# Kernel optimization log

Hardware: AMD Instinct MI355X
Metric: run time of the kernel (lower is better)

Reference implementation:

```python
import jax, jax.numpy as jnp
import numpy as np

P = 113          # modulus; eq_token = P, vocab = P + 1
D_MODEL = 1024
D_MLP = 4096
BATCH = 16384


def setup_inputs() -> dict:
    key = jax.random.key(0)
    ks = jax.random.split(key, 9)
    return {
        "a": jax.random.randint(ks[0], (BATCH,), 0, P, dtype=jnp.int64 if jax.config.jax_enable_x64 else jnp.int32),
        "b": jax.random.randint(ks[1], (BATCH,), 0, P, dtype=jnp.int64 if jax.config.jax_enable_x64 else jnp.int32),
        "token_embed": jax.random.normal(ks[2], (P + 1, D_MODEL), dtype=jnp.float32),
        "pos_embed": jax.random.normal(ks[3], (3, D_MODEL), dtype=jnp.float32),
        "W_in_w": jax.random.normal(ks[4], (D_MLP, D_MODEL), dtype=jnp.float32) * (1.0 / np.sqrt(D_MODEL)),
        "W_in_b": jax.random.normal(ks[5], (D_MLP,), dtype=jnp.float32) * 0.02,
        "W_out_w": jax.random.normal(ks[6], (D_MODEL, D_MLP), dtype=jnp.float32) * (1.0 / np.sqrt(D_MLP)),
        "W_out_b": jax.random.normal(ks[7], (D_MODEL,), dtype=jnp.float32) * 0.02,
        "unembed_w": jax.random.normal(ks[8], (P, D_MODEL), dtype=jnp.float32) * (1.0 / np.sqrt(D_MODEL)),
    }


def reference(a, b, token_embed, pos_embed, W_in_w, W_in_b, W_out_w, W_out_b, unembed_w):
    # tokens: (batch, 3) = [a, b, eq]
    eq = jnp.full_like(a, P)
    tokens = jnp.stack([a, b, eq], axis=1)
    # embed + positional: (batch, 3, d_model)
    x = token_embed[tokens] + pos_embed[None, :, :]
    # FNet-style mixing: FFT over seq (axis 1), then over d_model (axis 2), real part
    wave = jnp.fft.fft(jnp.fft.fft(x, axis=1), axis=2).real.astype(x.dtype)
    x = x + wave
    # MLP with residual
    h = jax.nn.relu(jnp.einsum('bsd,md->bsm', x, W_in_w) + W_in_b)
    x = x + jnp.einsum('bsm,dm->bsd', h, W_out_w) + W_out_b
    # unembed only the '=' position (index 2)
    logits = jnp.einsum('bd,vd->bv', x[:, 2, :], unembed_w)
    return logits
```

## Files before the change

kernel.cpp:

```cpp
#include <hip/hip_runtime.h>

typedef __attribute__((ext_vector_type(4))) float f32x4;
typedef __attribute__((ext_vector_type(8))) short short8;
typedef __attribute__((ext_vector_type(4))) unsigned short us4;

#define PMOD 113
#define NPAIR 12769
#define DM 1024
#define DMLP 4096
#define NBATCH 16384
#define SQRT3_2 0.86602540378443865f
#define CSTEP 6.1359231515425649e-3f
#define NZ 8
#define HPELEMS (228 * 4224)

__device__ __forceinline__ short f2bf(float x) {
    unsigned int u = __builtin_bit_cast(unsigned int, x);
    u += 0x7FFFu + ((u >> 16) & 1u);
    return (short)(u >> 16);
}
__device__ __forceinline__ float bf2f(short s) {
    return __builtin_bit_cast(float, (unsigned int)(unsigned short)s << 16);
}
__device__ __forceinline__ void cvt16(const float* p, short8& o0, short8& o1) {
    #pragma unroll
    for (int c4 = 0; c4 < 4; ++c4) {
        f32x4 v = *(const f32x4*)(p + c4 * 4);
        #pragma unroll
        for (int e = 0; e < 4; ++e) {
            short s = f2bf(v[e]);
            if (c4 < 2) o0[c4 * 4 + e] = s; else o1[(c4 - 2) * 4 + e] = s;
        }
    }
}

__global__ __launch_bounds__(256) void k_prep(
    unsigned short* __restrict__ Fb, unsigned short* __restrict__ V2b,
    unsigned short* __restrict__ Wob, unsigned short* __restrict__ Wib,
    unsigned short* __restrict__ Ub,
    const float* __restrict__ E, const float* __restrict__ pos,
    const float* __restrict__ Wo, const float* __restrict__ Wi,
    const float* __restrict__ U)
{
    __shared__ float smem[64 * 65];
    const int blk = blockIdx.x, tid = threadIdx.x;

    if (blk < 1024) {
        const int f = blk;
        for (int k = tid; k < DM; k += 256) {
            float v;
            if (k <= 512) v = cosf((float)((f * k) & 1023) * CSTEP);
            else          v = sinf((float)((f * (k - 512)) & 1023) * CSTEP);
            Fb[f * DM + k] = (unsigned short)f2bf(v);
        }
    } else if (blk < 1252) {
        const int t = blk - 1024;
        if (t >= 226) {
            for (int k = tid; k < DM; k += 256) V2b[t * DM + k] = 0;
            return;
        }
        float* vc = smem;
        float* vs = smem + 1024;
        if (t < PMOD) {
            const float* e = E + t * DM;
            const float* e2 = E + PMOD * DM;
            for (int d = tid; d < DM; d += 256) {
                float e2v = e2[d] + pos[2 * DM + d];
                vc[d] = e[d] + pos[d] - 0.5f * pos[DM + d] - 0.5f * e2v;
                vs[d] = SQRT3_2 * (pos[DM + d] - e2v);
            }
        } else {
            const float* e = E + (t - PMOD) * DM;
            for (int d = tid; d < DM; d += 256) {
                float x = e[d];
                vc[d] = -0.5f * x;
                vs[d] = SQRT3_2 * x;
            }
        }
        __syncthreads();
        for (int k = tid; k < DM; k += 256) {
            float o;
            if (k == 0)        o = vc[0];
            else if (k < 512)  o = vc[k] + vc[1024 - k];
            else if (k == 512) o = vc[512];
            else               o = vs[k - 512] - vs[1536 - k];
            V2b[t * DM + k] = (unsigned short)f2bf(o);
        }
    } else if (blk < 2276) {
        const int idx = blk - 1252;
        const int m0 = (idx & 63) * 64;
        const int d0 = (idx >> 6) * 64;
        float (*tile)[65] = (float(*)[65])smem;
        #pragma unroll
        for (int it = 0; it < 16; ++it) {
            int i2 = tid + it * 256;
            int r = i2 >> 6, c = i2 & 63;
            tile[c][r] = Wo[(d0 + r) * DMLP + m0 + c];
        }
        __syncthreads();
        #pragma unroll
        for (int it = 0; it < 16; ++it) {
            int i2 = tid + it * 256;
            int r = i2 >> 6, c = i2 & 63;
            Wob[(m0 + r) * DM + d0 + c] = (unsigned short)f2bf(tile[r][c]);
        }
    } else if (blk < 3300) {
        const int eb = (blk - 2276) * 4096 + tid * 16;
        short8 o0, o1;
        cvt16(Wi + eb, o0, o1);
        *(short8*)&Wib[eb] = o0;
        *(short8*)&Wib[eb + 8] = o1;
    } else {
        const int eb = (blk - 3300) * 4096 + tid * 16;
        if (eb < PMOD * DM) {
            short8 o0, o1;
            cvt16(U + eb, o0, o1);
            *(short8*)&Ub[eb] = o0;
            *(short8*)&Ub[eb + 8] = o1;
        }
    }
}

template<int MODE>
__device__ __forceinline__ void mfma_body(
    int n0, int row0, int kbeg, int kend, int Arows,
    unsigned short* __restrict__ C1, float* __restrict__ C2f,
    const unsigned short* __restrict__ A, const unsigned short* __restrict__ B1,
    const unsigned short* __restrict__ B2,
    const float* __restrict__ E, const float* __restrict__ pos,
    const float* __restrict__ bo, short* sA, short* sB)
{
    const int tid = threadIdx.x;
    const int sr = tid >> 2, sq = (tid & 3) * 16;
    const int lane = tid & 63, w = tid >> 6;
    const int wr = w >> 1, wc = w & 1;
    const int lr = lane & 15, lg = lane >> 4;

    const unsigned short* Ab = (row0 + sr < Arows) ? (A + (row0 + sr) * DM) : nullptr;
    const unsigned short* Bb;
    {
        int n = n0 + sr;
        if (MODE == 1) {
            if (n < 4096) Bb = B1 + n * DM;
            else if (n - 4096 < PMOD) Bb = B2 + (n - 4096) * DM;
            else Bb = nullptr;
        } else {
            Bb = B1 + n * DM;
        }
    }

    f32x4 acc[2][2];
    #pragma unroll
    for (int i = 0; i < 2; ++i)
        #pragma unroll
        for (int j = 0; j < 2; ++j) acc[i][j] = 0.f;

    for (int k0 = kbeg; k0 < kend; k0 += 64) {
        short8 a0, a1, b0, b1;
        if (Ab) { a0 = ((const short8*)(Ab + k0 + sq))[0];
                  a1 = ((const short8*)(Ab + k0 + sq))[1]; }
        else { a0 = 0; a1 = 0; }
        if (Bb) { b0 = ((const short8*)(Bb + k0 + sq))[0];
                  b1 = ((const short8*)(Bb + k0 + sq))[1]; }
        else { b0 = 0; b1 = 0; }
        if (k0 != kbeg) __syncthreads();
        *(short8*)&sA[sr * 72 + sq] = a0;
        *(short8*)&sA[sr * 72 + sq + 8] = a1;
        *(short8*)&sB[sr * 72 + sq] = b0;
        *(short8*)&sB[sr * 72 + sq + 8] = b1;
        __syncthreads();

        #pragma unroll
        for (int ks = 0; ks < 2; ++ks) {
            short8 af[2], bfr[2];
            #pragma unroll
            for (int i = 0; i < 2; ++i)
                af[i] = *(const short8*)&sA[(wr * 32 + i * 16 + lr) * 72 + ks * 32 + lg * 8];
            #pragma unroll
            for (int j = 0; j < 2; ++j)
                bfr[j] = *(const short8*)&sB[(wc * 32 + j * 16 + lr) * 72 + ks * 32 + lg * 8];
            #pragma unroll
            for (int i = 0; i < 2; ++i)
                #pragma unroll
                for (int j = 0; j < 2; ++j)
                    acc[i][j] = __builtin_amdgcn_mfma_f32_16x16x32_bf16(af[i], bfr[j], acc[i][j], 0, 0, 0);
        }
    }

    #pragma unroll
    for (int i = 0; i < 2; ++i) {
        #pragma unroll
        for (int q = 0; q < 4; ++q) {
            int r = row0 + wr * 32 + i * 16 + lg * 4 + q;
            #pragma unroll
            for (int j = 0; j < 2; ++j) {
                int cg = n0 + wc * 32 + j * 16 + lr;
                float v = acc[i][j][q];
                if (MODE == 0) {
                    if (r < 228) {
                        if (r < PMOD) v += E[PMOD * DM + cg] + pos[2 * DM + cg];
                        if (r == 227) v += bo[cg];
                        C1[r * DM + cg] = (unsigned short)f2bf(v);
                    }
                } else if (MODE == 1) {
                    if (r < 228) C2f[r * 4224 + cg] = v;
                } else {
                    if (r < 128) C1[r * DMLP + cg] = (unsigned short)f2bf(v);
                }
            }
        }
    }
}

__global__ __launch_bounds__(256) void k_m02(
    unsigned short* __restrict__ Tb, unsigned short* __restrict__ Mb,
    const unsigned short* __restrict__ V2b, const unsigned short* __restrict__ Fb,
    const unsigned short* __restrict__ Ub, const unsigned short* __restrict__ Wob,
    const float* __restrict__ E, const float* __restrict__ pos,
    const float* __restrict__ bo)
{
    __shared__ short sA[64 * 72];
    __shared__ short sB[64 * 72];
    const int blk = blockIdx.x;
    if (blk < 64) {
        mfma_body<0>((blk & 15) * 64, (blk >> 4) * 64, 0, DM, 228, Tb, nullptr,
                     V2b, Fb, nullptr, E, pos, bo, sA, sB);
    } else {
        int i = blk - 64;
        mfma_body<2>((i & 63) * 64, (i >> 6) * 64, 0, DM, PMOD, Mb, nullptr,
                     Ub, Wob, nullptr, nullptr, nullptr, nullptr, sA, sB);
    }
}

__global__ __launch_bounds__(256) void k_m1(
    float* __restrict__ Hp,
    const unsigned short* __restrict__ Tb, const unsigned short* __restrict__ Wib,
    const unsigned short* __restrict__ Ub)
{
    __shared__ short sA[64 * 72];
    __shared__ short sB[64 * 72];
    const int kbeg = blockIdx.z * 256;
    mfma_body<1>(blockIdx.x * 64, blockIdx.y * 64, kbeg, kbeg + 256, 228,
                 nullptr, Hp + (size_t)blockIdx.z * HPELEMS,
                 Tb, Wib, Ub, nullptr, nullptr, nullptr, sA, sB);
}

__global__ __launch_bounds__(256) void k_hred(
    unsigned short* __restrict__ Hb, float* __restrict__ L,
    const float* __restrict__ Hp, const float* __restrict__ bi)
{
    const int e = (blockIdx.x * 256 + threadIdx.x) * 4;
    if (e >= HPELEMS) return;
    f32x4 s = *(const f32x4*)(Hp + e);
    #pragma unroll
    for (int z = 1; z < 4; ++z) s += *(const f32x4*)(Hp + (size_t)z * HPELEMS + e);
    unsigned int row = (unsigned)e / 4224u;
    unsigned int col = (unsigned)e - row * 4224u;
    if (col < 4096) {
        if (row < PMOD) s += *(const f32x4*)(bi + col);
        us4 o;
        #pragma unroll
        for (int j = 0; j < 4; ++j) o[j] = (unsigned short)f2bf(s[j]);
        *(us4*)&Hb[row * DMLP + col] = o;
    } else {
        *(f32x4*)&L[row * 128 + (col - 4096)] = s;
    }
}

__global__ __launch_bounds__(256) void k_pair_gemm(
    unsigned short* __restrict__ LTp,
    const unsigned short* __restrict__ Hb,
    const unsigned short* __restrict__ Mb,
    const float* __restrict__ L)
{
    __shared__ short sH[128 * 72];
    __shared__ short sM[128 * 72];

    const int tid = threadIdx.x;
    const int p0 = blockIdx.x * 128;
    const int z = blockIdx.y;
    const int kbeg = z * 512;
    const bool slice0 = (z == 0);

    const int hr = tid >> 1, kh = (tid & 1) * 32;
    const unsigned int pc = (unsigned)min(p0 + hr, NPAIR - 1);
    const unsigned int a_r = pc / 113u;
    const unsigned int b_r = pc - a_r * 113u;
    const unsigned short* pHA = Hb + a_r * DMLP + kbeg + kh;
    const unsigned short* pHB = Hb + (PMOD + b_r) * DMLP + kbeg + kh;
    const unsigned short* pM  = Mb + hr * DMLP + kbeg + kh;

    const int lane = tid & 63, w = tid >> 6;
    const int wr = w >> 1, wc = w & 1;
    const int lr = lane & 15, lg = lane >> 4;

    f32x4 acc[4][4];
    #pragma unroll
    for (int i = 0; i < 4; ++i)
        #pragma unroll
        for (int j = 0; j < 4; ++j) acc[i][j] = 0.f;

    short8 rA[4], rB[4], rM[4];
    #pragma unroll
    for (int c = 0; c < 4; ++c) {
        rA[c] = *(const short8*)(pHA + c * 8);
        rB[c] = *(const short8*)(pHB + c * 8);
        rM[c] = *(const short8*)(pM + c * 8);
    }

    #pragma unroll 1
    for (int t = 0; t < 8; ++t) {
        short8 u[4];
        #pragma unroll
        for (int c = 0; c < 4; ++c)
            #pragma unroll
            for (int e = 0; e < 8; ++e)
                u[c][e] = f2bf(fmaxf(bf2f(rA[c][e]) + bf2f(rB[c][e]), 0.f));

        if (t) __syncthreads();
        #pragma unroll
        for (int c = 0; c < 4; ++c) {
            *(short8*)&sH[hr * 72 + kh + c * 8] = u[c];
            *(short8*)&sM[hr * 72 + kh + c * 8] = rM[c];
        }
        __syncthreads();

        if (t < 7) {
            #pragma unroll
            for (int c = 0; c < 4; ++c) {
                rA[c] = *(const short8*)(pHA + (t + 1) * 64 + c * 8);
                rB[c] = *(const short8*)(pHB + (t + 1) * 64 + c * 8);
                rM[c] = *(const short8*)(pM + (t + 1) * 64 + c * 8);
            }
        }

        #pragma unroll
        for (int ks = 0; ks < 2; ++ks) {
            short8 af[4], bf[4];
            #pragma unroll
            for (int i = 0; i < 4; ++i)
                af[i] = *(const short8*)&sH[(wr * 64 + i * 16 + lr) * 72 + ks * 32 + lg * 8];
            #pragma unroll
            for (int j = 0; j < 4; ++j)
                bf[j] = *(const short8*)&sM[(wc * 64 + j * 16 + lr) * 72 + ks * 32 + lg * 8];
            #pragma unroll
            for (int i = 0; i < 4; ++i)
                #pragma unroll
                for (int j = 0; j < 4; ++j)
                    acc[i][j] = __builtin_amdgcn_mfma_f32_16x16x32_bf16(af[i], bf[j], acc[i][j], 0, 0, 0);
        }
    }

    const float* Lb0 = L + PMOD * 128;
    const float* Lc = L + 227 * 128;
    #pragma unroll
    for (int i = 0; i < 4; ++i) {
        #pragma unroll
        for (int q = 0; q < 4; ++q) {
            int p = p0 + wr * 64 + i * 16 + lg * 4 + q;
            if (p >= NPAIR) continue;
            unsigned int pa = (unsigned)p / 113u;
            unsigned int pb = (unsigned)p - pa * 113u;
            unsigned short* dst = LTp + ((size_t)p * NZ + z) * 128;
            const float* La = L + pa * 128;
            const float* Lb = Lb0 + pb * 128;
            #pragma unroll
            for (int j = 0; j < 4; ++j) {
                int col = wc * 64 + j * 16 + lr;
                float val = acc[i][j][q];
                if (slice0) val += La[col] + Lb[col] + Lc[col];
                dst[col] = (unsigned short)f2bf(val);
            }
        }
    }
}

__global__ __launch_bounds__(256) void k_gather(
    float* __restrict__ out, const unsigned short* __restrict__ LTp,
    const int* __restrict__ a, const int* __restrict__ b)
{
    const int tid = threadIdx.x;
    const int elem = blockIdx.x * 16 + (tid >> 4);
    const int t16 = tid & 15;
    const int v0 = t16 * 8;
    if (v0 > 112) return;
    unsigned int pair = (unsigned)a[elem] * 113u + (unsigned)b[elem];
    const unsigned short* src = LTp + (size_t)pair * (NZ * 128) + v0;
    float s[8];
    #pragma unroll
    for (int e = 0; e < 8; ++e) s[e] = 0.f;
    #pragma unroll
    for (int z = 0; z < NZ; ++z) {
        short8 vv = *(const short8*)(src + z * 128);
        #pragma unroll
        for (int e = 0; e < 8; ++e) s[e] += bf2f(vv[e]);
    }
    float* o = out + (size_t)elem * PMOD + v0;
    const int nv = (v0 + 8 <= PMOD) ? 8 : (PMOD - v0);
    for (int e = 0; e < nv; ++e) o[e] = s[e];
}

extern "C" void kernel_launch(void* const* d_in, const int* in_sizes, int n_in,
                              void* d_out, int out_size, void* d_ws, size_t ws_size,
                              hipStream_t stream)
{
    const int*   a   = (const int*)d_in[0];
    const int*   b   = (const int*)d_in[1];
    const float* E   = (const float*)d_in[2];
    const float* pos = (const float*)d_in[3];
    const float* Wi  = (const float*)d_in[4];
    const float* bi  = (const float*)d_in[5];
    const float* Wo  = (const float*)d_in[6];
    const float* bo  = (const float*)d_in[7];
    const float* U   = (const float*)d_in[8];
    float* out = (float*)d_out;

    unsigned short* Fb  = (unsigned short*)d_ws;
    unsigned short* V2b = Fb + 1024 * 1024;
    unsigned short* Tb  = V2b + 228 * 1024;
    unsigned short* Hb  = Tb + 228 * 1024;
    unsigned short* Wob = Hb + 228 * 4096;
    unsigned short* Mb  = Wob + 4096 * 1024;
    unsigned short* Wib = Mb + 128 * 4096;
    unsigned short* Ub  = Wib + 4096 * 1024;
    unsigned short* LTp = Ub + 116 * 1024;
    float* L  = (float*)(LTp + (size_t)12800 * NZ * 128);
    float* Hp = L + 228 * 128;

    k_prep<<<3329, 256, 0, stream>>>(Fb, V2b, Wob, Wib, Ub, E, pos, Wo, Wi, U);
    k_m02<<<192, 256, 0, stream>>>(Tb, Mb, V2b, Fb, Ub, Wob, E, pos, bo);
    k_m1<<<dim3(66, 4, 4), 256, 0, stream>>>(Hp, Tb, Wib, Ub);
    k_hred<<<(HPELEMS / 4 + 255) / 256, 256, 0, stream>>>(Hb, L, Hp, bi);
    k_pair_gemm<<<dim3(100, NZ), 256, 0, stream>>>(LTp, Hb, Mb, L);
    k_gather<<<NBATCH / 16, 256, 0, stream>>>(out, LTp, a, b);

    (void)in_sizes; (void)n_in; (void)out_size; (void)ws_size;
}
```

Baseline: 171.6 us.

## Load M operand directly to registers, double-buffer H tile, truncate bf16 conversion

```diff
diff --git a/kernel.cpp b/kernel.cpp
--- a/kernel.cpp
+++ b/kernel.cpp
@@ -3,6 +3,7 @@
 typedef __attribute__((ext_vector_type(4))) float f32x4;
 typedef __attribute__((ext_vector_type(8))) short short8;
 typedef __attribute__((ext_vector_type(4))) unsigned short us4;
+typedef __attribute__((ext_vector_type(4))) unsigned int u32x4;
 
 #define PMOD 113
 #define NPAIR 12769
@@ -273,8 +274,7 @@
     const unsigned short* __restrict__ Mb,
     const float* __restrict__ L)
 {
-    __shared__ short sH[128 * 72];
-    __shared__ short sM[128 * 72];
+    __shared__ short sH[2][128 * 72];
 
     const int tid = threadIdx.x;
     const int p0 = blockIdx.x * 128;
@@ -288,66 +288,77 @@
     const unsigned int b_r = pc - a_r * 113u;
     const unsigned short* pHA = Hb + a_r * DMLP + kbeg + kh;
     const unsigned short* pHB = Hb + (PMOD + b_r) * DMLP + kbeg + kh;
-    const unsigned short* pM  = Mb + hr * DMLP + kbeg + kh;
 
     const int lane = tid & 63, w = tid >> 6;
     const int wr = w >> 1, wc = w & 1;
     const int lr = lane & 15, lg = lane >> 4;
 
+    const unsigned short* pM[4];
+    #pragma unroll
+    for (int j = 0; j < 4; ++j)
+        pM[j] = Mb + (wc * 64 + j * 16 + lr) * DMLP + kbeg + lg * 8;
+
     f32x4 acc[4][4];
     #pragma unroll
     for (int i = 0; i < 4; ++i)
         #pragma unroll
         for (int j = 0; j < 4; ++j) acc[i][j] = 0.f;
 
-    short8 rA[4], rB[4], rM[4];
+    short8 rA[4], rB[4];
     #pragma unroll
     for (int c = 0; c < 4; ++c) {
         rA[c] = *(const short8*)(pHA + c * 8);
         rB[c] = *(const short8*)(pHB + c * 8);
-        rM[c] = *(const short8*)(pM + c * 8);
     }
 
     #pragma unroll 1
     for (int t = 0; t < 8; ++t) {
+        short8 rM0[4], rM1[4];
+        #pragma unroll
+        for (int j = 0; j < 4; ++j) {
+            rM0[j] = *(const short8*)(pM[j] + t * 64);
+            rM1[j] = *(const short8*)(pM[j] + t * 64 + 32);
+        }
+
         short8 u[4];
         #pragma unroll
-        for (int c = 0; c < 4; ++c)
-            #pragma unroll
-            for (int e = 0; e < 8; ++e)
-                u[c][e] = f2bf(fmaxf(bf2f(rA[c][e]) + bf2f(rB[c][e]), 0.f));
-
-        if (t) __syncthreads();
-        #pragma unroll
         for (int c = 0; c < 4; ++c) {
-            *(short8*)&sH[hr * 72 + kh + c * 8] = u[c];
-            *(short8*)&sM[hr * 72 + kh + c * 8] = rM[c];
-        }
-        __syncthreads();
+            u32x4 up;
+            #pragma unroll
+            for (int e = 0; e < 4; ++e) {
+                float f0 = fmaxf(bf2f(rA[c][2 * e])     + bf2f(rB[c][2 * e]),     0.f);
+                float f1 = fmaxf(bf2f(rA[c][2 * e + 1]) + bf2f(rB[c][2 * e + 1]), 0.f);
+                up[e] = (__builtin_bit_cast(unsigned int, f1) & 0xffff0000u)
+                      | (__builtin_bit_cast(unsigned int, f0) >> 16);
+            }
+            u[c] = __builtin_bit_cast(short8, up);
+        }
 
         if (t < 7) {
             #pragma unroll
             for (int c = 0; c < 4; ++c) {
                 rA[c] = *(const short8*)(pHA + (t + 1) * 64 + c * 8);
                 rB[c] = *(const short8*)(pHB + (t + 1) * 64 + c * 8);
-                rM[c] = *(const short8*)(pM + (t + 1) * 64 + c * 8);
-            }
-        }
+            }
+        }
+
+        #pragma unroll
+        for (int c = 0; c < 4; ++c)
+            *(short8*)&sH[t & 1][hr * 72 + kh + c * 8] = u[c];
+        __syncthreads();
 
         #pragma unroll
         for (int ks = 0; ks < 2; ++ks) {
-            short8 af[4], bf[4];
+            short8 af[4];
             #pragma unroll
             for (int i = 0; i < 4; ++i)
-                af[i] = *(const short8*)&sH[(wr * 64 + i * 16 + lr) * 72 + ks * 32 + lg * 8];
-            #pragma unroll
-            for (int j = 0; j < 4; ++j)
-                bf[j] = *(const short8*)&sM[(wc * 64 + j * 16 + lr) * 72 + ks * 32 + lg * 8];
+                af[i] = *(const short8*)&sH[t & 1][(wr * 64 + i * 16 + lr) * 72 + ks * 32 + lg * 8];
             #pragma unroll
             for (int i = 0; i < 4; ++i)
                 #pragma unroll
                 for (int j = 0; j < 4; ++j)
-                    acc[i][j] = __builtin_amdgcn_mfma_f32_16x16x32_bf16(af[i], bf[j], acc[i][j], 0, 0, 0);
+                    acc[i][j] = __builtin_amdgcn_mfma_f32_16x16x32_bf16(
+                        af[i], ks ? rM1[j] : rM0[j], acc[i][j], 0, 0, 0);
         }
     }
 
```

After: 183.2 us. 6.7% more time.
